# Kernel optimization log

Measured on AMD Instinct MI355X. Metric: run time of the kernel, lower is better.

The kernel has to match this reference:

```python
import jax, jax.numpy as jnp
import numpy as np

N = 50000      # num_nodes
E = 300000     # edges per edge type
T = 3          # num_edge_type
C = 2          # num_channels
F_IN = 64      # feature_size
HID = 64       # hidden_size (w_out)
NL = 2         # num_layers (GT layers per FastGTN)
BETA = 0.5     # gtn_beta
TP = 0.8       # teleport_probability


def setup_inputs() -> dict:
    key = jax.random.key(0)
    ks = jax.random.split(key, 16)
    X = jax.random.normal(ks[0], (N, F_IN), dtype=jnp.float32)
    edge_index_0 = jax.random.randint(ks[1], (2, E), 0, N)
    edge_index_1 = jax.random.randint(ks[2], (2, E), 0, N)
    edge_index_2 = jax.random.randint(ks[3], (2, E), 0, N)
    edge_value_0 = jax.random.uniform(ks[4], (E,), dtype=jnp.float32)
    edge_value_1 = jax.random.uniform(ks[5], (E,), dtype=jnp.float32)
    edge_value_2 = jax.random.uniform(ks[6], (E,), dtype=jnp.float32)
    # glorot for Ws (per-channel projection), std=0.1 for GT layer mixing weights
    g0 = np.sqrt(6.0 / (F_IN + HID))
    g1 = np.sqrt(6.0 / (HID + HID))
    Ws0 = jax.random.uniform(ks[7], (C, F_IN, HID), minval=-g0, maxval=g0, dtype=jnp.float32)
    Ws1 = jax.random.uniform(ks[8], (C, HID, HID), minval=-g1, maxval=g1, dtype=jnp.float32)
    layerW0 = 0.1 * jax.random.normal(ks[9], (NL, C, T), dtype=jnp.float32)
    layerW1 = 0.1 * jax.random.normal(ks[10], (NL, C, T), dtype=jnp.float32)
    gl = np.sqrt(1.0 / (C * HID))
    lin_W0 = jax.random.uniform(ks[11], (C * HID, HID), minval=-gl, maxval=gl, dtype=jnp.float32)
    lin_b0 = jax.random.uniform(ks[12], (HID,), minval=-gl, maxval=gl, dtype=jnp.float32)
    lin_W1 = jax.random.uniform(ks[13], (C * HID, HID), minval=-gl, maxval=gl, dtype=jnp.float32)
    lin_b1 = jax.random.uniform(ks[14], (HID,), minval=-gl, maxval=gl, dtype=jnp.float32)
    return dict(X=X,
                edge_value_0=edge_value_0, edge_value_1=edge_value_1, edge_value_2=edge_value_2,
                Ws0=Ws0, Ws1=Ws1, layerW0=layerW0, layerW1=layerW1,
                lin_W0=lin_W0, lin_b0=lin_b0, lin_W1=lin_W1, lin_b1=lin_b1,
                edge_index_0=edge_index_0, edge_index_1=edge_index_1, edge_index_2=edge_index_2)


def _spmm_mix(H, filt, vals, etype, row, col):
    # H: [C, N, d]; filt: [C, T] softmaxed; vals: [Etot]; etype/row/col: [Etot]
    # == for each channel c: sum_j filt[c,j] * (A_j @ H[c])
    w = vals[None, :] * filt[:, etype]          # [C, Etot]
    msg = w[:, :, None] * H[:, col, :]          # [C, Etot, d]
    return jax.vmap(lambda m: jax.ops.segment_sum(m, row, num_segments=N))(msg)


def _fastgtn_block(Xin, Ws, layerW, linW, linb, row, col, vals, etype):
    H = jnp.einsum('nf,cfo->cno', Xin, Ws)      # [C, N, HID]
    X0 = jax.lax.stop_gradient(H)               # X_ = H.clone().detach()
    for l in range(NL):
        filt = jax.nn.softmax(layerW[l], axis=1)
        H = _spmm_mix(H, filt, vals, etype, row, col)
    Hm = TP * jax.nn.relu(BETA * X0 + (1.0 - BETA) * H) + (1.0 - TP) * X0
    Hm = jnp.transpose(Hm, (1, 0, 2)).reshape(N, C * Hm.shape[-1])  # [N, C*HID]
    return jax.nn.relu(Hm @ linW + linb)


def reference(X, edge_value_0, edge_value_1, edge_value_2,
              Ws0, Ws1, layerW0, layerW1,
              lin_W0, lin_b0, lin_W1, lin_b1,
              edge_index_0, edge_index_1, edge_index_2):
    row = jnp.concatenate([edge_index_0[0], edge_index_1[0], edge_index_2[0]])
    col = jnp.concatenate([edge_index_0[1], edge_index_1[1], edge_index_2[1]])
    vals = jnp.concatenate([edge_value_0, edge_value_1, edge_value_2])
    etype = jnp.repeat(jnp.arange(T), E)
    H = _fastgtn_block(X, Ws0, layerW0, lin_W0, lin_b0, row, col, vals, etype)
    H = _fastgtn_block(H, Ws1, layerW1, lin_W1, lin_b1, row, col, vals, etype)
    return H
```

## Files before the change

kernel.cpp:

```cpp
#include <hip/hip_runtime.h>
#include <hip/hip_fp16.h>

#define NN 50000
#define EE 300000
#define ETOT (3 * EE)
#define HD 64
#define SCAN_BLOCKS ((NN + 1023) / 1024)


__global__ void filt_kernel(const float* __restrict__ lw0,
                            const float* __restrict__ lw1,
                            float* __restrict__ filt) {
    int i = threadIdx.x;
    if (i < 8) {
        int b = i >> 2, l = (i >> 1) & 1, c = i & 1;
        const float* lw = (b == 0 ? lw0 : lw1) + l * 6 + c * 3;
        float a0 = lw[0], a1 = lw[1], a2 = lw[2];
        float m  = fmaxf(a0, fmaxf(a1, a2));
        float e0 = expf(a0 - m), e1 = expf(a1 - m), e2 = expf(a2 - m);
        float s  = e0 + e1 + e2;
        float* o = filt + i * 3;
        o[0] = e0 / s; o[1] = e1 / s; o[2] = e2 / s;
    }
}

__global__ void __launch_bounds__(256)
hist_kernel(const int* __restrict__ ei0, const int* __restrict__ ei1,
            const int* __restrict__ ei2, int* __restrict__ cnt) {
    int t = blockIdx.y;
    const int* ei = (t == 0) ? ei0 : (t == 1) ? ei1 : ei2;
    int e = blockIdx.x * 256 + threadIdx.x;
    if (e < EE) atomicAdd(&cnt[ei[e]], 1);
}

__global__ void __launch_bounds__(1024)
scanA_kernel(const int* __restrict__ cnt, int* __restrict__ incl,
             int* __restrict__ bsum) {
    __shared__ int wsum[16];
    int tid = threadIdx.x;
    int i = blockIdx.x * 1024 + tid;
    int lane = tid & 63, wv = tid >> 6;
    int v = (i < NN) ? cnt[i] : 0;
    int x = v;
#pragma unroll
    for (int d = 1; d < 64; d <<= 1) {
        int y = __shfl_up(x, d);
        if (lane >= d) x += y;
    }
    if (lane == 63) wsum[wv] = x;
    __syncthreads();
    if (wv == 0 && lane < 16) {
        int y = wsum[lane];
#pragma unroll
        for (int d = 1; d < 16; d <<= 1) {
            int z = __shfl_up(y, d);
            if (lane >= d) y += z;
        }
        wsum[lane] = y;
    }
    __syncthreads();
    if (wv > 0) x += wsum[wv - 1];
    if (i < NN) incl[i] = x;
    if (tid == 1023) bsum[blockIdx.x] = x;
}

__global__ void __launch_bounds__(64)
scanB_kernel(int* __restrict__ bsum) {
    int lane = threadIdx.x;
    int v = (lane < SCAN_BLOCKS) ? bsum[lane] : 0;
    int x = v;
#pragma unroll
    for (int d = 1; d < 64; d <<= 1) {
        int y = __shfl_up(x, d);
        if (lane >= d) x += y;
    }
    if (lane < SCAN_BLOCKS) bsum[lane] = x - v;
}

__global__ void __launch_bounds__(1024)
scanC_kernel(const int* __restrict__ cnt, const int* __restrict__ incl,
             const int* __restrict__ bsum, int* __restrict__ rp,
             int* __restrict__ cursor) {
    int i = blockIdx.x * 1024 + threadIdx.x;
    if (i < NN) {
        int total = incl[i] + bsum[blockIdx.x];
        rp[i + 1] = total;
        cursor[i] = total - cnt[i];
    }
    if (i == 0) rp[0] = 0;
}

__global__ void __launch_bounds__(256)
scatter_kernel(const int* __restrict__ ei0, const int* __restrict__ ei1,
               const int* __restrict__ ei2,
               const float* __restrict__ ev0, const float* __restrict__ ev1,
               const float* __restrict__ ev2,
               int* __restrict__ cursor, unsigned int* __restrict__ meta) {
    int t = blockIdx.y;
    const int*   ei = (t == 0) ? ei0 : (t == 1) ? ei1 : ei2;
    const float* ev = (t == 0) ? ev0 : (t == 1) ? ev1 : ev2;
    int e = blockIdx.x * 256 + threadIdx.x;
    if (e >= EE) return;
    int row = ei[e];
    int col = ei[EE + e];
    unsigned int q = (unsigned int)__float2int_rn(ev[e] * 16383.0f);
    int pos = atomicAdd(&cursor[row], 1);
    meta[pos] = (unsigned int)col | ((unsigned int)t << 16) | (q << 18);
}

#define PROJ_NTILE (NN / 16)
__global__ void __launch_bounds__(256)
proj_kernel(const float* __restrict__ Xin, const float* __restrict__ Ws,
            __half2* __restrict__ Hh) {
    __shared__ float Wl[2 * 64 * 64];
    __shared__ float Xs[16 * 65];
    int tid = threadIdx.x;
    for (int i = tid; i < 2 * 64 * 64; i += 256) Wl[i] = Ws[i];
    int oq = (tid & 15) * 4;
    int ln = tid >> 4;
    for (int tile = blockIdx.x; tile < PROJ_NTILE; tile += gridDim.x) {
        int n0 = tile * 16;
        __syncthreads();
        for (int i = tid; i < 16 * 64; i += 256)
            Xs[(i >> 6) * 65 + (i & 63)] = Xin[(n0 + (i >> 6)) * 64 + (i & 63)];
        __syncthreads();
        float a0[4] = {0.f, 0.f, 0.f, 0.f};
        float a1[4] = {0.f, 0.f, 0.f, 0.f};
        for (int f = 0; f < 64; ++f) {
            float  x  = Xs[ln * 65 + f];
            float4 w0 = *(const float4*)&Wl[f * 64 + oq];
            float4 w1 = *(const float4*)&Wl[4096 + f * 64 + oq];
            a0[0] += x * w0.x; a0[1] += x * w0.y;
            a0[2] += x * w0.z; a0[3] += x * w0.w;
            a1[0] += x * w1.x; a1[1] += x * w1.y;
            a1[2] += x * w1.z; a1[3] += x * w1.w;
        }
        float4 o4;
        ((__half2*)&o4)[0] = __floats2half2_rn(a0[0], a1[0]);
        ((__half2*)&o4)[1] = __floats2half2_rn(a0[1], a1[1]);
        ((__half2*)&o4)[2] = __floats2half2_rn(a0[2], a1[2]);
        ((__half2*)&o4)[3] = __floats2half2_rn(a0[3], a1[3]);
        *(float4*)&Hh[(n0 + ln) * HD + oq] = o4;
    }
}

__global__ void __launch_bounds__(256)
spmm_kernel(const float4* __restrict__ Hin4, float4* __restrict__ Hout4,
            const unsigned int* __restrict__ meta, const int* __restrict__ rp,
            const float* __restrict__ filt ) {
    const int wid  = threadIdx.x >> 6;
    const int lane = threadIdx.x & 63;
    const int g    = lane >> 4;
    const int fq   = lane & 15;
    const int row  = blockIdx.x * 4 + wid;

    const float s = 1.0f / 16383.0f;
    const float F00 = filt[0] * s, F01 = filt[1] * s, F02 = filt[2] * s;
    const float F10 = filt[3] * s, F11 = filt[4] * s, F12 = filt[5] * s;

    float accA[4] = {0.f, 0.f, 0.f, 0.f};
    float accB[4] = {0.f, 0.f, 0.f, 0.f};

    const int beg = rp[row], end = rp[row + 1];
    for (int j0 = beg; j0 < end; j0 += 64) {
        int cnt = min(end - j0, 64);
        unsigned int m = (lane < cnt) ? meta[j0 + lane] : 0u;
        for (int k = 0; k < cnt; k += 8) {
            unsigned int mmA = (unsigned int)__shfl((int)m, k + g);
            unsigned int mmB = (unsigned int)__shfl((int)m, k + 4 + g);
            float4 rA = Hin4[(mmA & 0xffffu) * 16 + fq];
            float4 rB = Hin4[(mmB & 0xffffu) * 16 + fq];
            int   etA = (mmA >> 16) & 3,  etB = (mmB >> 16) & 3;
            float qA  = (float)(mmA >> 18), qB = (float)(mmB >> 18);
            float w0A = qA * ((etA == 0) ? F00 : (etA == 1) ? F01 : F02);
            float w1A = qA * ((etA == 0) ? F10 : (etA == 1) ? F11 : F12);
            float w0B = qB * ((etB == 0) ? F00 : (etB == 1) ? F01 : F02);
            float w1B = qB * ((etB == 0) ? F10 : (etB == 1) ? F11 : F12);
#pragma unroll
            for (int i = 0; i < 4; ++i) {
                float2 xA = __half22float2(((const __half2*)&rA)[i]);
                float2 xB = __half22float2(((const __half2*)&rB)[i]);
                accA[i] += w0A * xA.x + w0B * xB.x;
                accB[i] += w1A * xA.y + w1B * xB.y;
            }
        }
    }
#pragma unroll
    for (int i = 0; i < 4; ++i) {
        accA[i] += __shfl_xor(accA[i], 16); accA[i] += __shfl_xor(accA[i], 32);
        accB[i] += __shfl_xor(accB[i], 16); accB[i] += __shfl_xor(accB[i], 32);
    }
    if (g == 0) {
        float4 o4;
        ((__half2*)&o4)[0] = __floats2half2_rn(accA[0], accB[0]);
        ((__half2*)&o4)[1] = __floats2half2_rn(accA[1], accB[1]);
        ((__half2*)&o4)[2] = __floats2half2_rn(accA[2], accB[2]);
        ((__half2*)&o4)[3] = __floats2half2_rn(accA[3], accB[3]);
        Hout4[row * 16 + fq] = o4;
    }
}

#define EPI_TILE 64
#define HS_STRIDE 132
__global__ void __launch_bounds__(256)
epilogue_kernel(const __half2* __restrict__ X0, const __half2* __restrict__ H,
                const float* __restrict__ linW, const float* __restrict__ linb,
                float* __restrict__ out) {
    __shared__ float Wl[128 * 64];
    __shared__ float Hs[EPI_TILE * HS_STRIDE];
    int tid = threadIdx.x;
    for (int i = tid; i < 128 * 64; i += 256) Wl[i] = linW[i];
    int oq = tid & 15, nq = tid >> 4;
    float bias[4];
#pragma unroll
    for (int i = 0; i < 4; ++i) bias[i] = linb[oq + 16 * i];
    const int ntiles = (NN + EPI_TILE - 1) / EPI_TILE;
    for (int tile = blockIdx.x; tile < ntiles; tile += gridDim.x) {
        int n0 = tile * EPI_TILE;
        __syncthreads();
        for (int i = tid; i < EPI_TILE * 64; i += 256) {
            int ln = i >> 6, d = i & 63;
            int n = n0 + ln;
            float2 x0 = make_float2(0.f, 0.f), h = make_float2(0.f, 0.f);
            if (n < NN) {
                x0 = __half22float2(X0[n * HD + d]);
                h  = __half22float2(H [n * HD + d]);
            }
            float z0 = fmaxf(0.5f * x0.x + 0.5f * h.x, 0.f);
            float z1 = fmaxf(0.5f * x0.y + 0.5f * h.y, 0.f);
            Hs[ln * HS_STRIDE + d]      = 0.8f * z0 + 0.2f * x0.x;
            Hs[ln * HS_STRIDE + 64 + d] = 0.8f * z1 + 0.2f * x0.y;
        }
        __syncthreads();
        float acc[4][4];
#pragma unroll
        for (int j = 0; j < 4; ++j)
#pragma unroll
            for (int i = 0; i < 4; ++i) acc[j][i] = bias[i];
        for (int k = 0; k < 128; k += 4) {
            float4 hq[4];
#pragma unroll
            for (int j = 0; j < 4; ++j)
                hq[j] = *(const float4*)&Hs[(nq + 16 * j) * HS_STRIDE + k];
#pragma unroll
            for (int kk = 0; kk < 4; ++kk) {
                float w[4];
#pragma unroll
                for (int i = 0; i < 4; ++i) w[i] = Wl[(k + kk) * 64 + oq + 16 * i];
#pragma unroll
                for (int j = 0; j < 4; ++j) {
                    float x = (kk == 0) ? hq[j].x : (kk == 1) ? hq[j].y
                             : (kk == 2) ? hq[j].z : hq[j].w;
#pragma unroll
                    for (int i = 0; i < 4; ++i) acc[j][i] += x * w[i];
                }
            }
        }
#pragma unroll
        for (int j = 0; j < 4; ++j) {
            int n = n0 + nq + 16 * j;
            if (n < NN) {
#pragma unroll
                for (int i = 0; i < 4; ++i)
                    out[n * HD + oq + 16 * i] = fmaxf(acc[j][i], 0.f);
            }
        }
    }
}

extern "C" void kernel_launch(void* const* d_in, const int* in_sizes, int n_in,
                              void* d_out, int out_size, void* d_ws, size_t ws_size,
                              hipStream_t stream) {
    const float* X     = (const float*)d_in[0];
    const float* ev0   = (const float*)d_in[1];
    const float* ev1   = (const float*)d_in[2];
    const float* ev2   = (const float*)d_in[3];
    const float* Ws0   = (const float*)d_in[4];
    const float* Ws1   = (const float*)d_in[5];
    const float* lw0   = (const float*)d_in[6];
    const float* lw1   = (const float*)d_in[7];
    const float* linW0 = (const float*)d_in[8];
    const float* linb0 = (const float*)d_in[9];
    const float* linW1 = (const float*)d_in[10];
    const float* linb1 = (const float*)d_in[11];
    const int*   ei0   = (const int*)d_in[12];
    const int*   ei1   = (const int*)d_in[13];
    const int*   ei2   = (const int*)d_in[14];
    float* out = (float*)d_out;

    float* ws = (float*)d_ws;
    __half2* X0h = (__half2*)(ws);
    __half2* Ha  = (__half2*)(ws + 1 * NN * HD);
    __half2* Hb  = (__half2*)(ws + 2 * NN * HD);
    float*   mid = ws + 3 * NN * HD;
    float*   filt = ws + 4 * NN * HD;
    int*     cnt    = (int*)(filt + 32);
    int*     incl   = cnt + NN;
    int*     bsum   = incl + NN;
    int*     rp     = bsum + 64;
    int*     cursor = rp + NN + 1;
    unsigned int* meta = (unsigned int*)(cursor + NN);

    filt_kernel<<<1, 64, 0, stream>>>(lw0, lw1, filt);
    hipMemsetAsync(cnt, 0, NN * sizeof(int), stream);
    dim3 egrid((EE + 255) / 256, 3);
    hist_kernel<<<egrid, 256, 0, stream>>>(ei0, ei1, ei2, cnt);
    scanA_kernel<<<SCAN_BLOCKS, 1024, 0, stream>>>(cnt, incl, bsum);
    scanB_kernel<<<1, 64, 0, stream>>>(bsum);
    scanC_kernel<<<SCAN_BLOCKS, 1024, 0, stream>>>(cnt, incl, bsum, rp, cursor);
    scatter_kernel<<<egrid, 256, 0, stream>>>(ei0, ei1, ei2, ev0, ev1, ev2,
                                              cursor, meta);

    proj_kernel<<<512, 256, 0, stream>>>(X, Ws0, X0h);
    spmm_kernel<<<NN / 4, 256, 0, stream>>>((const float4*)X0h, (float4*)Ha,
                                            meta, rp, filt + 0);
    spmm_kernel<<<NN / 4, 256, 0, stream>>>((const float4*)Ha, (float4*)Hb,
                                            meta, rp, filt + 6);
    epilogue_kernel<<<512, 256, 0, stream>>>(X0h, Hb, linW0, linb0, mid);

    proj_kernel<<<512, 256, 0, stream>>>(mid, Ws1, X0h);
    spmm_kernel<<<NN / 4, 256, 0, stream>>>((const float4*)X0h, (float4*)Ha,
                                            meta, rp, filt + 12);
    spmm_kernel<<<NN / 4, 256, 0, stream>>>((const float4*)Ha, (float4*)Hb,
                                            meta, rp, filt + 18);
    epilogue_kernel<<<512, 256, 0, stream>>>(X0h, Hb, linW1, linb1, out);
}
```

Before: 436.5 us.

## Build CSR via two-level binning by row block instead of global hist-scan-scatter

Replaces the per-row histogram, three-kernel scan and global atomic scatter with a two-level approach. Edges are first binned into 196 buckets of 256 rows each, using one padded atomic counter per bucket, and staged in the mid buffer. A single-block scan then computes the bucket offsets. Finally, one block per bucket does a local shared-memory histogram, scan and scatter, then writes meta coalesced. This cuts kernel launches and spreads atomics over shared memory, but relies on a fixed per-bucket capacity of 6144 staged edges, which could overflow on skewed inputs.

```diff
diff --git a/kernel.cpp b/kernel.cpp
--- a/kernel.cpp
+++ b/kernel.cpp
@@ -5,7 +5,9 @@
 #define EE 300000
 #define ETOT (3 * EE)
 #define HD 64
-#define SCAN_BLOCKS ((NN + 1023) / 1024)
+#define RB 256
+#define NB 196
+#define BSTRIDE 6144
 
 
 __global__ void filt_kernel(const float* __restrict__ lw0,
@@ -25,77 +27,11 @@
 }
 
 __global__ void __launch_bounds__(256)
-hist_kernel(const int* __restrict__ ei0, const int* __restrict__ ei1,
-            const int* __restrict__ ei2, int* __restrict__ cnt) {
-    int t = blockIdx.y;
-    const int* ei = (t == 0) ? ei0 : (t == 1) ? ei1 : ei2;
-    int e = blockIdx.x * 256 + threadIdx.x;
-    if (e < EE) atomicAdd(&cnt[ei[e]], 1);
-}
-
-__global__ void __launch_bounds__(1024)
-scanA_kernel(const int* __restrict__ cnt, int* __restrict__ incl,
-             int* __restrict__ bsum) {
-    __shared__ int wsum[16];
-    int tid = threadIdx.x;
-    int i = blockIdx.x * 1024 + tid;
-    int lane = tid & 63, wv = tid >> 6;
-    int v = (i < NN) ? cnt[i] : 0;
-    int x = v;
-#pragma unroll
-    for (int d = 1; d < 64; d <<= 1) {
-        int y = __shfl_up(x, d);
-        if (lane >= d) x += y;
-    }
-    if (lane == 63) wsum[wv] = x;
-    __syncthreads();
-    if (wv == 0 && lane < 16) {
-        int y = wsum[lane];
-#pragma unroll
-        for (int d = 1; d < 16; d <<= 1) {
-            int z = __shfl_up(y, d);
-            if (lane >= d) y += z;
-        }
-        wsum[lane] = y;
-    }
-    __syncthreads();
-    if (wv > 0) x += wsum[wv - 1];
-    if (i < NN) incl[i] = x;
-    if (tid == 1023) bsum[blockIdx.x] = x;
-}
-
-__global__ void __launch_bounds__(64)
-scanB_kernel(int* __restrict__ bsum) {
-    int lane = threadIdx.x;
-    int v = (lane < SCAN_BLOCKS) ? bsum[lane] : 0;
-    int x = v;
-#pragma unroll
-    for (int d = 1; d < 64; d <<= 1) {
-        int y = __shfl_up(x, d);
-        if (lane >= d) x += y;
-    }
-    if (lane < SCAN_BLOCKS) bsum[lane] = x - v;
-}
-
-__global__ void __launch_bounds__(1024)
-scanC_kernel(const int* __restrict__ cnt, const int* __restrict__ incl,
-             const int* __restrict__ bsum, int* __restrict__ rp,
-             int* __restrict__ cursor) {
-    int i = blockIdx.x * 1024 + threadIdx.x;
-    if (i < NN) {
-        int total = incl[i] + bsum[blockIdx.x];
-        rp[i + 1] = total;
-        cursor[i] = total - cnt[i];
-    }
-    if (i == 0) rp[0] = 0;
-}
-
-__global__ void __launch_bounds__(256)
-scatter_kernel(const int* __restrict__ ei0, const int* __restrict__ ei1,
-               const int* __restrict__ ei2,
-               const float* __restrict__ ev0, const float* __restrict__ ev1,
-               const float* __restrict__ ev2,
-               int* __restrict__ cursor, unsigned int* __restrict__ meta) {
+bin_kernel(const int* __restrict__ ei0, const int* __restrict__ ei1,
+           const int* __restrict__ ei2,
+           const float* __restrict__ ev0, const float* __restrict__ ev1,
+           const float* __restrict__ ev2,
+           int* __restrict__ cursor, uint2* __restrict__ staged) {
     int t = blockIdx.y;
     const int*   ei = (t == 0) ? ei0 : (t == 1) ? ei1 : ei2;
     const float* ev = (t == 0) ? ev0 : (t == 1) ? ev1 : ev2;
@@ -104,8 +40,85 @@
     int row = ei[e];
     int col = ei[EE + e];
     unsigned int q = (unsigned int)__float2int_rn(ev[e] * 16383.0f);
-    int pos = atomicAdd(&cursor[row], 1);
-    meta[pos] = (unsigned int)col | ((unsigned int)t << 16) | (q << 18);
+    unsigned int mw = (unsigned int)col | ((unsigned int)t << 16) | (q << 18);
+    int b = row >> 8;
+    int pos = atomicAdd(&cursor[b * 16], 1);
+    staged[b * BSTRIDE + pos] = make_uint2(mw, (unsigned int)row);
+}
+
+__global__ void __launch_bounds__(256)
+bscan_kernel(const int* __restrict__ cursor, int* __restrict__ bbase,
+             int* __restrict__ rp) {
+    __shared__ int wsum[4];
+    int tid = threadIdx.x, lane = tid & 63, wv = tid >> 6;
+    int v = (tid < NB) ? cursor[tid * 16] : 0;
+    int x = v;
+#pragma unroll
+    for (int d = 1; d < 64; d <<= 1) {
+        int y = __shfl_up(x, d);
+        if (lane >= d) x += y;
+    }
+    if (lane == 63) wsum[wv] = x;
+    __syncthreads();
+    if (tid == 0) {
+        int s = 0;
+        for (int i = 0; i < 4; ++i) { int t = wsum[i]; wsum[i] = s; s += t; }
+    }
+    __syncthreads();
+    x += wsum[wv];
+    if (tid < NB) bbase[tid] = x - v;
+    if (tid == 0) rp[NN] = ETOT;
+}
+
+__global__ void __launch_bounds__(256)
+csr_kernel(const uint2* __restrict__ staged, const int* __restrict__ cursor,
+           const int* __restrict__ bbase, int* __restrict__ rp,
+           unsigned int* __restrict__ meta) {
+    __shared__ int hist[RB];
+    __shared__ int lcur[RB];
+    __shared__ int wsum[4];
+    __shared__ unsigned int metaL[BSTRIDE];
+    int b   = blockIdx.x;
+    int tid = threadIdx.x;
+    int cnt  = cursor[b * 16];
+    int base = bbase[b];
+    int row0 = b * RB;
+
+    hist[tid] = 0;
+    __syncthreads();
+    for (int i = tid; i < cnt; i += 256) {
+        uint2 s = staged[b * BSTRIDE + i];
+        atomicAdd(&hist[(int)s.y - row0], 1);
+    }
+    __syncthreads();
+    int lane = tid & 63, wv = tid >> 6;
+    int v = hist[tid];
+    int x = v;
+#pragma unroll
+    for (int d = 1; d < 64; d <<= 1) {
+        int y = __shfl_up(x, d);
+        if (lane >= d) x += y;
+    }
+    if (lane == 63) wsum[wv] = x;
+    __syncthreads();
+    if (tid == 0) {
+        int s = 0;
+        for (int i = 0; i < 4; ++i) { int t = wsum[i]; wsum[i] = s; s += t; }
+    }
+    __syncthreads();
+    int excl = x + wsum[wv] - v;
+    lcur[tid] = excl;
+    int row = row0 + tid;
+    if (row < NN) rp[row] = base + excl;
+    __syncthreads();
+    for (int i = tid; i < cnt; i += 256) {
+        uint2 s = staged[b * BSTRIDE + i];
+        int p = atomicAdd(&lcur[(int)s.y - row0], 1);
+        metaL[p] = s.x;
+    }
+    __syncthreads();
+    for (int i = tid; i < cnt; i += 256)
+        meta[base + i] = metaL[i];
 }
 
 #define PROJ_NTILE (NN / 16)
@@ -293,23 +306,20 @@
     __half2* Ha  = (__half2*)(ws + 1 * NN * HD);
     __half2* Hb  = (__half2*)(ws + 2 * NN * HD);
     float*   mid = ws + 3 * NN * HD;
-    float*   filt = ws + 4 * NN * HD;
-    int*     cnt    = (int*)(filt + 32);
-    int*     incl   = cnt + NN;
-    int*     bsum   = incl + NN;
-    int*     rp     = bsum + 64;
-    int*     cursor = rp + NN + 1;
-    unsigned int* meta = (unsigned int*)(cursor + NN);
+    uint2*   staged = (uint2*)mid;
+    float*   filt   = ws + 4 * NN * HD;
+    int*     cursor = (int*)(filt + 32);
+    int*     bbase  = cursor + NB * 16;
+    int*     rp     = bbase + 256;
+    unsigned int* meta = (unsigned int*)(rp + NN + 16);
 
     filt_kernel<<<1, 64, 0, stream>>>(lw0, lw1, filt);
-    hipMemsetAsync(cnt, 0, NN * sizeof(int), stream);
+    hipMemsetAsync(cursor, 0, NB * 16 * sizeof(int), stream);
     dim3 egrid((EE + 255) / 256, 3);
-    hist_kernel<<<egrid, 256, 0, stream>>>(ei0, ei1, ei2, cnt);
-    scanA_kernel<<<SCAN_BLOCKS, 1024, 0, stream>>>(cnt, incl, bsum);
-    scanB_kernel<<<1, 64, 0, stream>>>(bsum);
-    scanC_kernel<<<SCAN_BLOCKS, 1024, 0, stream>>>(cnt, incl, bsum, rp, cursor);
-    scatter_kernel<<<egrid, 256, 0, stream>>>(ei0, ei1, ei2, ev0, ev1, ev2,
-                                              cursor, meta);
+    bin_kernel<<<egrid, 256, 0, stream>>>(ei0, ei1, ei2, ev0, ev1, ev2,
+                                          cursor, staged);
+    bscan_kernel<<<1, 256, 0, stream>>>(cursor, bbase, rp);
+    csr_kernel<<<NB, 256, 0, stream>>>(staged, cursor, bbase, rp, meta);
 
     proj_kernel<<<512, 256, 0, stream>>>(X, Ws0, X0h);
     spmm_kernel<<<NN / 4, 256, 0, stream>>>((const float4*)X0h, (float4*)Ha,
```

Measured after the change: 443.0 us. Within noise of the previous version (+1.5%).
